# Kernel tuning notes

Hardware: AMD Instinct MI355X
Metric: run time of the kernel (lower is better)

## Reference

```python
import jax, jax.numpy as jnp
import numpy as np

B, S, D = 8, 1024, 1024
NEG = -1e9


def setup_inputs() -> dict:
    key = jax.random.key(0)
    ks = jax.random.split(key, 6)
    context = jax.random.normal(ks[0], (B, S, D), dtype=jnp.float32)
    eos_mask = jax.random.randint(ks[1], (B, S, S), 0, 2).astype(jnp.int32)
    scale = 1.0 / np.sqrt(D).astype(np.float32)
    Wq = jax.random.normal(ks[2], (D, D), dtype=jnp.float32) * scale
    bq = jnp.zeros((D,), jnp.float32)
    Wk = jax.random.normal(ks[3], (D, D), dtype=jnp.float32) * scale
    bk = jnp.zeros((D,), jnp.float32)
    ln_a = jnp.ones((D,), jnp.float32)
    ln_b = jnp.zeros((D,), jnp.float32)
    return dict(context=context, eos_mask=eos_mask, Wq=Wq, bq=bq, Wk=Wk, bk=bk,
                ln_a=ln_a, ln_b=ln_b)


def _forward(context, eos_mask, Wq, bq, Wk, bk, ln_a, ln_b):
    d_model = context.shape[-1]
    seq_len = context.shape[1]
    # LayerNorm with torch-style unbiased std (ddof=1)
    mean = context.mean(-1, keepdims=True)
    var = ((context - mean) ** 2).sum(-1, keepdims=True) / (d_model - 1)
    x = ln_a * (context - mean) / (jnp.sqrt(var) + 1e-6) + ln_b

    a = jnp.eye(seq_len, k=1, dtype=jnp.int32)    # super-diagonal
    b = jnp.eye(seq_len, k=0, dtype=jnp.int32)    # diagonal
    c = jnp.eye(seq_len, k=-1, dtype=jnp.int32)   # sub-diagonal
    tri = jnp.triu(jnp.ones((seq_len, seq_len), jnp.float32), 0)

    mask = eos_mask & (a + c)  # [B,S,S] banded + eos mask

    q = x @ Wq.T + bq
    k = x @ Wk.T + bk
    scores = jnp.einsum('bsd,btd->bst', q, k) / d_model
    scores = jnp.where(mask == 0, NEG, scores)
    neibor = jax.nn.softmax(scores, axis=-1)
    neibor = jnp.sqrt(neibor * jnp.swapaxes(neibor, -2, -1) + 1e-9)

    # log-space triangular matmul 'scan'
    t = jnp.where(a == 0, 0.0, jnp.log(neibor + 1e-9)) @ tri  # [B,S,S]
    g = jnp.exp(jnp.einsum('st,btu->bsu', tri, t))
    strict_upper = tri.astype(jnp.int32) - b
    g = jnp.where(strict_upper == 0, 0.0, g)
    g = g + jnp.swapaxes(g, -2, -1) + jnp.where(b == 0, 1e-9, neibor)
    return g, neibor


def reference(context, eos_mask, Wq, bq, Wk, bk, ln_a, ln_b):
    return _forward(context, eos_mask, Wq, bq, Wk, bk, ln_a, ln_b)
```

## Files before the change

### kernel.cpp

```cpp
#include <hip/hip_runtime.h>
#include <math.h>

#define B_ 8
#define S_ 1024
#define D_ 1024
constexpr int BS = B_ * S_;

typedef short bf16x8 __attribute__((ext_vector_type(8)));
typedef float f32x4 __attribute__((ext_vector_type(4)));

__device__ __forceinline__ unsigned short f2bf(float f) {
    unsigned int u = __float_as_uint(f);
    u += 0x7fffu + ((u >> 16) & 1u);
    return (unsigned short)(u >> 16);
}
__device__ __forceinline__ float bf2f(unsigned short h) {
    return __uint_as_float(((unsigned int)h) << 16);
}

__device__ __forceinline__ float block_reduce_sum(float val, float* sh) {
    int tid = threadIdx.x;
    int lane = tid & 63, w = tid >> 6;
    #pragma unroll
    for (int off = 32; off > 0; off >>= 1) val += __shfl_down(val, off, 64);
    if (lane == 0) sh[w] = val;
    __syncthreads();
    int nw = blockDim.x >> 6;
    float total = 0.f;
    for (int i = 0; i < nw; i++) total += sh[i];
    __syncthreads();
    return total;
}

__global__ void ln_kernel(const float* __restrict__ ctx,
                          const float* __restrict__ ln_a,
                          const float* __restrict__ ln_b,
                          unsigned short* __restrict__ xb) {
    __shared__ float sh[4];
    int r = blockIdx.x;
    int tid = threadIdx.x;
    const float* row = ctx + (size_t)r * D_;
    float v[4];
    float s = 0.f;
    #pragma unroll
    for (int i = 0; i < 4; i++) { v[i] = row[tid + i * 256]; s += v[i]; }
    float total = block_reduce_sum(s, sh);
    float mean = total * (1.0f / D_);
    float sq = 0.f;
    #pragma unroll
    for (int i = 0; i < 4; i++) { float d = v[i] - mean; sq += d * d; }
    float varsum = block_reduce_sum(sq, sh);
    float var = varsum * (1.0f / (D_ - 1));
    float inv = 1.0f / (sqrtf(var) + 1e-6f);
    unsigned short* orow = xb + (size_t)r * D_;
    #pragma unroll
    for (int i = 0; i < 4; i++) {
        int d = tid + i * 256;
        orow[d] = f2bf(ln_a[d] * (v[i] - mean) * inv + ln_b[d]);
    }
}

__global__ void transpose_bf16(const float* __restrict__ in,
                               unsigned short* __restrict__ out, int n) {
    __shared__ float t[32][33];
    int bx = blockIdx.x * 32, by = blockIdx.y * 32;
    int tx = threadIdx.x, ty = threadIdx.y;
    #pragma unroll
    for (int i = 0; i < 32; i += 8)
        t[ty + i][tx] = in[(size_t)(by + ty + i) * n + bx + tx];
    __syncthreads();
    #pragma unroll
    for (int i = 0; i < 32; i += 8)
        out[(size_t)(bx + ty + i) * n + by + tx] = f2bf(t[tx][ty + i]);
}

__global__ __launch_bounds__(256) void gemm_bt(
    const unsigned short* __restrict__ A,
    const unsigned short* __restrict__ Bt,
    unsigned short* __restrict__ C,
    int M, int N, int K) {
    __shared__ __align__(16) unsigned short As[128 * 64];
    __shared__ __align__(16) unsigned short Bs[128 * 64];
    const int tid = threadIdx.x;
    const int wave = tid >> 6, lane = tid & 63;
    const int bm = blockIdx.y * 128, bn = blockIdx.x * 128;
    const int lrow8 = lane >> 3;
    const int pchunk = lane & 7;
    const int m_lane = lane & 15, quad = lane >> 4;
    const int wr = wave >> 1, wc = wave & 1;

    f32x4 acc[4][4] = {};

    for (int k0 = 0; k0 < K; k0 += 64) {
        #pragma unroll
        for (int c = 0; c < 4; c++) {
            int row = wave * 32 + c * 8 + lrow8;
            int gchunk = pchunk ^ (row & 7);
            const unsigned short* gpA = A + (size_t)(bm + row) * K + k0 + gchunk * 8;
            const unsigned short* gpB = Bt + (size_t)(bn + row) * K + k0 + gchunk * 8;
            __builtin_amdgcn_global_load_lds(
                (const __attribute__((address_space(1))) void*)gpA,
                (__attribute__((address_space(3))) void*)(As + (wave * 32 + c * 8) * 64),
                16, 0, 0);
            __builtin_amdgcn_global_load_lds(
                (const __attribute__((address_space(1))) void*)gpB,
                (__attribute__((address_space(3))) void*)(Bs + (wave * 32 + c * 8) * 64),
                16, 0, 0);
        }
        __syncthreads();
        #pragma unroll
        for (int kk = 0; kk < 2; kk++) {
            bf16x8 af[4], bfr[4];
            #pragma unroll
            for (int i = 0; i < 4; i++) {
                int row = wr * 64 + i * 16 + m_lane;
                int lchunk = kk * 4 + quad;
                af[i] = *(const bf16x8*)(As + row * 64 + (lchunk ^ (row & 7)) * 8);
            }
            #pragma unroll
            for (int j = 0; j < 4; j++) {
                int row = wc * 64 + j * 16 + m_lane;
                int lchunk = kk * 4 + quad;
                bfr[j] = *(const bf16x8*)(Bs + row * 64 + (lchunk ^ (row & 7)) * 8);
            }
            #pragma unroll
            for (int i = 0; i < 4; i++)
                #pragma unroll
                for (int j = 0; j < 4; j++)
                    acc[i][j] = __builtin_amdgcn_mfma_f32_16x16x32_bf16(
                        af[i], bfr[j], acc[i][j], 0, 0, 0);
        }
        __syncthreads();
    }
    #pragma unroll
    for (int i = 0; i < 4; i++)
        #pragma unroll
        for (int j = 0; j < 4; j++)
            #pragma unroll
            for (int r = 0; r < 4; r++) {
                int row = bm + wr * 64 + i * 16 + quad * 4 + r;
                int col = bn + wc * 64 + j * 16 + m_lane;
                C[(size_t)row * N + col] = f2bf(acc[i][j][r]);
            }
}

__global__ void bias_terms(const float* __restrict__ Wq, const float* __restrict__ Wk,
                           const float* __restrict__ bq, const float* __restrict__ bk,
                           float* __restrict__ u, float* __restrict__ v,
                           float* __restrict__ c0) {
    __shared__ float sh[4];
    int col = blockIdx.x;
    int tid = threadIdx.x;
    float s = 0.f;
    if (col < D_) {
        for (int d = tid; d < D_; d += 256) s += Wk[(size_t)d * D_ + col] * bq[d];
        s = block_reduce_sum(s, sh);
        if (tid == 0) u[col] = s;
    } else if (col < 2 * D_) {
        int c = col - D_;
        for (int d = tid; d < D_; d += 256) s += Wq[(size_t)d * D_ + c] * bk[d];
        s = block_reduce_sum(s, sh);
        if (tid == 0) v[c] = s;
    } else {
        for (int d = tid; d < D_; d += 256) s += bq[d] * bk[d];
        s = block_reduce_sum(s, sh);
        if (tid == 0) *c0 = s;
    }
}

__global__ void band_dots(const unsigned short* __restrict__ Y,
                          const unsigned short* __restrict__ X,
                          const float* __restrict__ u, const float* __restrict__ v,
                          float* __restrict__ ydu, float* __restrict__ ydd,
                          float* __restrict__ au, float* __restrict__ av) {
    __shared__ float sh[4];
    int r = blockIdx.x;
    int s = r & (S_ - 1);
    int tid = threadIdx.x;
    bool has_up = (s < S_ - 1), has_dn = (s > 0);
    const unsigned short* yrow = Y + (size_t)r * D_;
    const unsigned short* xrow = X + (size_t)r * D_;
    const unsigned short* xup = X + (size_t)(r + 1) * D_;
    const unsigned short* xdn = X + (size_t)(r - 1) * D_;
    int d0 = tid * 4;
    ushort4 yv4 = *(const ushort4*)(yrow + d0);
    ushort4 xv4 = *(const ushort4*)(xrow + d0);
    ushort4 xu4 = has_up ? *(const ushort4*)(xup + d0) : make_ushort4(0, 0, 0, 0);
    ushort4 xd4 = has_dn ? *(const ushort4*)(xdn + d0) : make_ushort4(0, 0, 0, 0);
    float4 uv = *(const float4*)(u + d0);
    float4 vv = *(const float4*)(v + d0);
    float s_up = 0, s_dn = 0, s_u = 0, s_v = 0;
    {
        float y0 = bf2f(yv4.x), y1 = bf2f(yv4.y), y2 = bf2f(yv4.z), y3 = bf2f(yv4.w);
        float x0 = bf2f(xv4.x), x1 = bf2f(xv4.y), x2 = bf2f(xv4.z), x3 = bf2f(xv4.w);
        s_up = y0 * bf2f(xu4.x) + y1 * bf2f(xu4.y) + y2 * bf2f(xu4.z) + y3 * bf2f(xu4.w);
        s_dn = y0 * bf2f(xd4.x) + y1 * bf2f(xd4.y) + y2 * bf2f(xd4.z) + y3 * bf2f(xd4.w);
        s_u = uv.x * x0 + uv.y * x1 + uv.z * x2 + uv.w * x3;
        s_v = vv.x * x0 + vv.y * x1 + vv.z * x2 + vv.w * x3;
    }
    s_up = block_reduce_sum(s_up, sh);
    s_dn = block_reduce_sum(s_dn, sh);
    s_u  = block_reduce_sum(s_u, sh);
    s_v  = block_reduce_sum(s_v, sh);
    if (tid == 0) { ydu[r] = s_up; ydd[r] = s_dn; au[r] = s_u; av[r] = s_v; }
}

__global__ void softmax_band(const float* __restrict__ ydu, const float* __restrict__ ydd,
                             const float* __restrict__ au, const float* __restrict__ av,
                             const float* __restrict__ c0p, const int* __restrict__ eos,
                             float* __restrict__ Pup, float* __restrict__ Pdn,
                             float* __restrict__ bg) {
    int r = blockIdx.x * blockDim.x + threadIdx.x;
    if (r >= BS) return;
    int b = r >> 10, s = r & (S_ - 1);
    float c0 = *c0p;
    const float inv_d = 1.0f / D_;
    bool mu = false, md = false;
    float su = 0.f, sd = 0.f;
    if (s < S_ - 1) {
        mu = eos[(size_t)b * S_ * S_ + (size_t)s * S_ + (s + 1)] != 0;
        su = (ydu[r] + av[r] + au[r + 1] + c0) * inv_d;
    }
    if (s > 0) {
        md = eos[(size_t)b * S_ * S_ + (size_t)s * S_ + (s - 1)] != 0;
        sd = (ydd[r] + av[r] + au[r - 1] + c0) * inv_d;
    }
    float pu, pd, pb;
    if (mu && md) {
        float m = fmaxf(su, sd);
        float eu = expf(su - m), ed = expf(sd - m);
        float inv = 1.0f / (eu + ed);
        pu = eu * inv; pd = ed * inv; pb = 0.f;
    } else if (mu) { pu = 1.f; pd = 0.f; pb = 0.f; }
    else if (md)   { pu = 0.f; pd = 1.f; pb = 0.f; }
    else           { pu = pd = pb = 1.0f / S_; }
    Pup[r] = pu; Pdn[r] = pd; bg[r] = pb;
}

__global__ void prefix_kernel(const float* __restrict__ Pup, const float* __restrict__ Pdn,
                              double* __restrict__ C) {
    __shared__ double wsum[16];
    int b = blockIdx.x;
    int t = threadIdx.x;
    size_t base = (size_t)b * S_;
    double l = 0.0;
    if (t < S_ - 1) {
        float p = sqrtf(Pup[base + t] * Pdn[base + t + 1] + 1e-9f) + 1e-9f;
        l = log((double)p);
    }
    int lane = t & 63, w = t >> 6;
    double v = l;
    #pragma unroll
    for (int off = 1; off < 64; off <<= 1) {
        double o = __shfl_up(v, off, 64);
        if (lane >= off) v += o;
    }
    if (lane == 63) wsum[w] = v;
    __syncthreads();
    if (t == 0) {
        double acc = 0.0;
        #pragma unroll
        for (int i = 0; i < 16; i++) { double x = wsum[i]; wsum[i] = acc; acc += x; }
    }
    __syncthreads();
    v += wsum[w];
    if (t == 0) C[base] = 0.0;
    if (t < S_ - 1) C[base + t + 1] = v;
}

__global__ void write_out(const float* __restrict__ Pup, const float* __restrict__ Pdn,
                          const float* __restrict__ bg, const double* __restrict__ C,
                          float* __restrict__ out) {
    int r = blockIdx.x;
    int b = r >> 10, s = r & (S_ - 1);
    size_t rowbase = (size_t)r * S_;
    size_t bb = (size_t)b * S_;
    float pu_s = (s < S_ - 1) ? Pup[r] : 0.f;
    float pd_s = (s > 0) ? Pdn[r] : 0.f;
    float bg_s = bg[r];
    double C_s = C[r];
    int t0 = threadIdx.x * 4;
    float* gp = out;
    float* np = out + (size_t)B_ * S_ * S_;
    float4 gv, nv;
    #pragma unroll
    for (int j = 0; j < 4; j++) {
        int t = t0 + j;
        float P_st = (t == s + 1) ? pu_s : ((t == s - 1) ? pd_s : bg_s);
        float P_ts;
        if (t == s - 1)      P_ts = Pup[bb + t];
        else if (t == s + 1) P_ts = Pdn[bb + t];
        else                 P_ts = bg[bb + t];
        float neib = sqrtf(P_st * P_ts + 1e-9f);
        float g;
        if (t == s) {
            g = neib;
        } else {
            double diff = (t > s) ? (C[bb + t] - C_s) : (C_s - C[bb + t]);
            g = expf((float)diff) + 1e-9f;
        }
        ((float*)&gv)[j] = g;
        ((float*)&nv)[j] = neib;
    }
    *(float4*)(gp + rowbase + t0) = gv;
    *(float4*)(np + rowbase + t0) = nv;
}

extern "C" void kernel_launch(void* const* d_in, const int* in_sizes, int n_in,
                              void* d_out, int out_size, void* d_ws, size_t ws_size,
                              hipStream_t stream) {
    const float* ctx  = (const float*)d_in[0];
    const int*   eos  = (const int*)d_in[1];
    const float* Wq   = (const float*)d_in[2];
    const float* bq   = (const float*)d_in[3];
    const float* Wk   = (const float*)d_in[4];
    const float* bk   = (const float*)d_in[5];
    const float* ln_a = (const float*)d_in[6];
    const float* ln_b = (const float*)d_in[7];
    float* out = (float*)d_out;

    char* ws = (char*)d_ws;
    size_t off = 0;
    auto alloc = [&](size_t bytes) {
        void* p = ws + off;
        off += (bytes + 255) & ~(size_t)255;
        return p;
    };
    unsigned short* Xb  = (unsigned short*)alloc((size_t)BS * D_ * 2);
    unsigned short* Wqt = (unsigned short*)alloc((size_t)D_ * D_ * 2);
    unsigned short* Wkt = (unsigned short*)alloc((size_t)D_ * D_ * 2);
    unsigned short* Mt  = (unsigned short*)alloc((size_t)D_ * D_ * 2);
    unsigned short* Yb  = (unsigned short*)alloc((size_t)BS * D_ * 2);
    float*  u   = (float*)alloc(D_ * 4);
    float*  v   = (float*)alloc(D_ * 4);
    float*  c0  = (float*)alloc(4);
    float*  ydu = (float*)alloc(BS * 4);
    float*  ydd = (float*)alloc(BS * 4);
    float*  au  = (float*)alloc(BS * 4);
    float*  av  = (float*)alloc(BS * 4);
    float*  Pup = (float*)alloc(BS * 4);
    float*  Pdn = (float*)alloc(BS * 4);
    float*  bg  = (float*)alloc(BS * 4);
    double* Cp  = (double*)alloc(BS * 8);

    ln_kernel<<<BS, 256, 0, stream>>>(ctx, ln_a, ln_b, Xb);
    transpose_bf16<<<dim3(32, 32), dim3(32, 8), 0, stream>>>(Wq, Wqt, D_);
    transpose_bf16<<<dim3(32, 32), dim3(32, 8), 0, stream>>>(Wk, Wkt, D_);
    gemm_bt<<<dim3(8, 8), 256, 0, stream>>>(Wkt, Wqt, Mt, D_, D_, D_);
    bias_terms<<<2 * D_ + 1, 256, 0, stream>>>(Wq, Wk, bq, bk, u, v, c0);
    gemm_bt<<<dim3(8, 64), 256, 0, stream>>>(Xb, Mt, Yb, BS, D_, D_);
    band_dots<<<BS, 256, 0, stream>>>(Yb, Xb, u, v, ydu, ydd, au, av);
    softmax_band<<<BS / 256, 256, 0, stream>>>(ydu, ydd, au, av, c0, eos, Pup, Pdn, bg);
    prefix_kernel<<<B_, 1024, 0, stream>>>(Pup, Pdn, Cp);
    write_out<<<BS, 256, 0, stream>>>(Pup, Pdn, bg, Cp, out);
}
```

Measured before the change: 231.4 us.

## Fuse band dot products into GEMM epilogue and merge small kernels

The big X·M GEMM now computes the banded dot products (Y row against neighbouring X rows, plus the u/v bias terms) in its epilogue. It reduces them with shuffles and atomics, so the bf16 Y intermediate is no longer written and re-read. The two weight transposes share one launch, and bias_terms becomes a row-parallel accumulation with atomics. The weight-product GEMM uses 64x64 tiles for more blocks, and softmax and prefix are merged into one kernel. The atomics need a memset up front, and the epilogue performs scattered global reads of X.

Result: faster. 217.8 us (-5.9%).

```diff
diff --git a/kernel.cpp b/kernel.cpp
--- a/kernel.cpp
+++ b/kernel.cpp
@@ -60,24 +60,127 @@
     }
 }
 
-__global__ void transpose_bf16(const float* __restrict__ in,
-                               unsigned short* __restrict__ out, int n) {
+__global__ void transpose2_bf16(const float* __restrict__ inq,
+                                const float* __restrict__ ink,
+                                unsigned short* __restrict__ outq,
+                                unsigned short* __restrict__ outk) {
     __shared__ float t[32][33];
+    const float* in = blockIdx.z ? ink : inq;
+    unsigned short* out = blockIdx.z ? outk : outq;
     int bx = blockIdx.x * 32, by = blockIdx.y * 32;
     int tx = threadIdx.x, ty = threadIdx.y;
     #pragma unroll
     for (int i = 0; i < 32; i += 8)
-        t[ty + i][tx] = in[(size_t)(by + ty + i) * n + bx + tx];
+        t[ty + i][tx] = in[(size_t)(by + ty + i) * D_ + bx + tx];
     __syncthreads();
     #pragma unroll
     for (int i = 0; i < 32; i += 8)
-        out[(size_t)(bx + ty + i) * n + by + tx] = f2bf(t[tx][ty + i]);
-}
-
-__global__ __launch_bounds__(256) void gemm_bt(
+        out[(size_t)(bx + ty + i) * D_ + by + tx] = f2bf(t[tx][ty + i]);
+}
+
+__global__ void bias_terms(const float* __restrict__ Wq, const float* __restrict__ Wk,
+                           const float* __restrict__ bq, const float* __restrict__ bk,
+                           float* __restrict__ u, float* __restrict__ v,
+                           float* __restrict__ c0) {
+    int b = blockIdx.x;
+    int tid = threadIdx.x;
+    float ua[4] = {}, va[4] = {};
+    int d0 = b * 128;
+    for (int d = d0; d < d0 + 128; d++) {
+        float bqd = bq[d], bkd = bk[d];
+        const float* wkr = Wk + (size_t)d * D_;
+        const float* wqr = Wq + (size_t)d * D_;
+        #pragma unroll
+        for (int i = 0; i < 4; i++) {
+            int c = tid + i * 256;
+            ua[i] += wkr[c] * bqd;
+            va[i] += wqr[c] * bkd;
+        }
+    }
+    #pragma unroll
+    for (int i = 0; i < 4; i++) {
+        atomicAdd(&u[tid + i * 256], ua[i]);
+        atomicAdd(&v[tid + i * 256], va[i]);
+    }
+    if (tid < 128) atomicAdd(c0, bq[d0 + tid] * bk[d0 + tid]);
+}
+
+__global__ __launch_bounds__(256) void gemm_bt64(
     const unsigned short* __restrict__ A,
     const unsigned short* __restrict__ Bt,
     unsigned short* __restrict__ C,
+    int M, int N, int K) {
+    __shared__ __align__(16) unsigned short As[64 * 64];
+    __shared__ __align__(16) unsigned short Bs[64 * 64];
+    const int tid = threadIdx.x;
+    const int wave = tid >> 6, lane = tid & 63;
+    const int bm = blockIdx.y * 64, bn = blockIdx.x * 64;
+    const int lrow8 = lane >> 3;
+    const int pchunk = lane & 7;
+    const int m_lane = lane & 15, quad = lane >> 4;
+    const int wr = wave >> 1, wc = wave & 1;
+
+    f32x4 acc[2][2] = {};
+
+    for (int k0 = 0; k0 < K; k0 += 64) {
+        #pragma unroll
+        for (int c = 0; c < 2; c++) {
+            int row = wave * 16 + c * 8 + lrow8;
+            int gchunk = pchunk ^ (row & 7);
+            const unsigned short* gpA = A + (size_t)(bm + row) * K + k0 + gchunk * 8;
+            const unsigned short* gpB = Bt + (size_t)(bn + row) * K + k0 + gchunk * 8;
+            __builtin_amdgcn_global_load_lds(
+                (const __attribute__((address_space(1))) void*)gpA,
+                (__attribute__((address_space(3))) void*)(As + (wave * 16 + c * 8) * 64),
+                16, 0, 0);
+            __builtin_amdgcn_global_load_lds(
+                (const __attribute__((address_space(1))) void*)gpB,
+                (__attribute__((address_space(3))) void*)(Bs + (wave * 16 + c * 8) * 64),
+                16, 0, 0);
+        }
+        __syncthreads();
+        #pragma unroll
+        for (int kk = 0; kk < 2; kk++) {
+            bf16x8 af[2], bfr[2];
+            #pragma unroll
+            for (int i = 0; i < 2; i++) {
+                int row = wr * 32 + i * 16 + m_lane;
+                int lchunk = kk * 4 + quad;
+                af[i] = *(const bf16x8*)(As + row * 64 + (lchunk ^ (row & 7)) * 8);
+            }
+            #pragma unroll
+            for (int j = 0; j < 2; j++) {
+                int row = wc * 32 + j * 16 + m_lane;
+                int lchunk = kk * 4 + quad;
+                bfr[j] = *(const bf16x8*)(Bs + row * 64 + (lchunk ^ (row & 7)) * 8);
+            }
+            #pragma unroll
+            for (int i = 0; i < 2; i++)
+                #pragma unroll
+                for (int j = 0; j < 2; j++)
+                    acc[i][j] = __builtin_amdgcn_mfma_f32_16x16x32_bf16(
+                        af[i], bfr[j], acc[i][j], 0, 0, 0);
+        }
+        __syncthreads();
+    }
+    #pragma unroll
+    for (int i = 0; i < 2; i++)
+        #pragma unroll
+        for (int j = 0; j < 2; j++)
+            #pragma unroll
+            for (int r = 0; r < 4; r++) {
+                int row = bm + wr * 32 + i * 16 + quad * 4 + r;
+                int col = bn + wc * 32 + j * 16 + m_lane;
+                C[(size_t)row * N + col] = f2bf(acc[i][j][r]);
+            }
+}
+
+__global__ __launch_bounds__(256) void gemm_fused(
+    const unsigned short* __restrict__ A,
+    const unsigned short* __restrict__ Bt,
+    const float* __restrict__ u, const float* __restrict__ v,
+    float* __restrict__ ydu, float* __restrict__ ydd,
+    float* __restrict__ au, float* __restrict__ av,
     int M, int N, int K) {
     __shared__ __align__(16) unsigned short As[128 * 64];
     __shared__ __align__(16) unsigned short Bs[128 * 64];
@@ -132,97 +235,72 @@
         }
         __syncthreads();
     }
-    #pragma unroll
-    for (int i = 0; i < 4; i++)
-        #pragma unroll
-        for (int j = 0; j < 4; j++)
-            #pragma unroll
-            for (int r = 0; r < 4; r++) {
-                int row = bm + wr * 64 + i * 16 + quad * 4 + r;
-                int col = bn + wc * 64 + j * 16 + m_lane;
-                C[(size_t)row * N + col] = f2bf(acc[i][j][r]);
-            }
-}
-
-__global__ void bias_terms(const float* __restrict__ Wq, const float* __restrict__ Wk,
-                           const float* __restrict__ bq, const float* __restrict__ bk,
-                           float* __restrict__ u, float* __restrict__ v,
-                           float* __restrict__ c0) {
-    __shared__ float sh[4];
-    int col = blockIdx.x;
-    int tid = threadIdx.x;
-    float s = 0.f;
-    if (col < D_) {
-        for (int d = tid; d < D_; d += 256) s += Wk[(size_t)d * D_ + col] * bq[d];
-        s = block_reduce_sum(s, sh);
-        if (tid == 0) u[col] = s;
-    } else if (col < 2 * D_) {
-        int c = col - D_;
-        for (int d = tid; d < D_; d += 256) s += Wq[(size_t)d * D_ + c] * bk[d];
-        s = block_reduce_sum(s, sh);
-        if (tid == 0) v[c] = s;
-    } else {
-        for (int d = tid; d < D_; d += 256) s += bq[d] * bk[d];
-        s = block_reduce_sum(s, sh);
-        if (tid == 0) *c0 = s;
-    }
-}
-
-__global__ void band_dots(const unsigned short* __restrict__ Y,
-                          const unsigned short* __restrict__ X,
-                          const float* __restrict__ u, const float* __restrict__ v,
-                          float* __restrict__ ydu, float* __restrict__ ydd,
-                          float* __restrict__ au, float* __restrict__ av) {
-    __shared__ float sh[4];
-    int r = blockIdx.x;
-    int s = r & (S_ - 1);
-    int tid = threadIdx.x;
-    bool has_up = (s < S_ - 1), has_dn = (s > 0);
-    const unsigned short* yrow = Y + (size_t)r * D_;
-    const unsigned short* xrow = X + (size_t)r * D_;
-    const unsigned short* xup = X + (size_t)(r + 1) * D_;
-    const unsigned short* xdn = X + (size_t)(r - 1) * D_;
-    int d0 = tid * 4;
-    ushort4 yv4 = *(const ushort4*)(yrow + d0);
-    ushort4 xv4 = *(const ushort4*)(xrow + d0);
-    ushort4 xu4 = has_up ? *(const ushort4*)(xup + d0) : make_ushort4(0, 0, 0, 0);
-    ushort4 xd4 = has_dn ? *(const ushort4*)(xdn + d0) : make_ushort4(0, 0, 0, 0);
-    float4 uv = *(const float4*)(u + d0);
-    float4 vv = *(const float4*)(v + d0);
-    float s_up = 0, s_dn = 0, s_u = 0, s_v = 0;
-    {
-        float y0 = bf2f(yv4.x), y1 = bf2f(yv4.y), y2 = bf2f(yv4.z), y3 = bf2f(yv4.w);
-        float x0 = bf2f(xv4.x), x1 = bf2f(xv4.y), x2 = bf2f(xv4.z), x3 = bf2f(xv4.w);
-        s_up = y0 * bf2f(xu4.x) + y1 * bf2f(xu4.y) + y2 * bf2f(xu4.z) + y3 * bf2f(xu4.w);
-        s_dn = y0 * bf2f(xd4.x) + y1 * bf2f(xd4.y) + y2 * bf2f(xd4.z) + y3 * bf2f(xd4.w);
-        s_u = uv.x * x0 + uv.y * x1 + uv.z * x2 + uv.w * x3;
-        s_v = vv.x * x0 + vv.y * x1 + vv.z * x2 + vv.w * x3;
-    }
-    s_up = block_reduce_sum(s_up, sh);
-    s_dn = block_reduce_sum(s_dn, sh);
-    s_u  = block_reduce_sum(s_u, sh);
-    s_v  = block_reduce_sum(s_v, sh);
-    if (tid == 0) { ydu[r] = s_up; ydd[r] = s_dn; au[r] = s_u; av[r] = s_v; }
-}
-
-__global__ void softmax_band(const float* __restrict__ ydu, const float* __restrict__ ydd,
-                             const float* __restrict__ au, const float* __restrict__ av,
-                             const float* __restrict__ c0p, const int* __restrict__ eos,
-                             float* __restrict__ Pup, float* __restrict__ Pdn,
-                             float* __restrict__ bg) {
-    int r = blockIdx.x * blockDim.x + threadIdx.x;
-    if (r >= BS) return;
-    int b = r >> 10, s = r & (S_ - 1);
+
+    int cols[4];
+    float uvals[4], vvals[4];
+    #pragma unroll
+    for (int j = 0; j < 4; j++) {
+        cols[j] = bn + wc * 64 + j * 16 + m_lane;
+        uvals[j] = u[cols[j]];
+        vvals[j] = v[cols[j]];
+    }
+    #pragma unroll
+    for (int i = 0; i < 4; i++) {
+        #pragma unroll
+        for (int r = 0; r < 4; r++) {
+            int lrow = wr * 64 + i * 16 + quad * 4 + r;
+            int row = bm + lrow;
+            int s = row & (S_ - 1);
+            bool hu = (s < S_ - 1), hd = (s > 0);
+            const unsigned short* xc = A + (size_t)row * D_;
+            float pu = 0.f, pd = 0.f, pau = 0.f, pav = 0.f;
+            #pragma unroll
+            for (int j = 0; j < 4; j++) {
+                int c = cols[j];
+                float a = acc[i][j][r];
+                float xv = bf2f(xc[c]);
+                if (hu) pu += a * bf2f(xc[c + D_]);
+                if (hd) pd += a * bf2f(xc[c - D_]);
+                pau += uvals[j] * xv;
+                pav += vvals[j] * xv;
+            }
+            #pragma unroll
+            for (int off = 1; off < 16; off <<= 1) {
+                pu += __shfl_xor(pu, off, 64);
+                pd += __shfl_xor(pd, off, 64);
+                pau += __shfl_xor(pau, off, 64);
+                pav += __shfl_xor(pav, off, 64);
+            }
+            if (m_lane == 0) {
+                atomicAdd(&ydu[row], pu);
+                atomicAdd(&ydd[row], pd);
+                atomicAdd(&au[row], pau);
+                atomicAdd(&av[row], pav);
+            }
+        }
+    }
+}
+
+__global__ void softmax_prefix(const float* __restrict__ ydu, const float* __restrict__ ydd,
+                               const float* __restrict__ au, const float* __restrict__ av,
+                               const float* __restrict__ c0p, const int* __restrict__ eos,
+                               float* __restrict__ Pup, float* __restrict__ Pdn,
+                               float* __restrict__ bg, double* __restrict__ C) {
+    __shared__ float pdsh[1024];
+    __shared__ double wsum[16];
+    int b = blockIdx.x;
+    int t = threadIdx.x;
+    int r = b * S_ + t;
     float c0 = *c0p;
     const float inv_d = 1.0f / D_;
     bool mu = false, md = false;
     float su = 0.f, sd = 0.f;
-    if (s < S_ - 1) {
-        mu = eos[(size_t)b * S_ * S_ + (size_t)s * S_ + (s + 1)] != 0;
+    if (t < S_ - 1) {
+        mu = eos[(size_t)b * S_ * S_ + (size_t)t * S_ + (t + 1)] != 0;
         su = (ydu[r] + av[r] + au[r + 1] + c0) * inv_d;
     }
-    if (s > 0) {
-        md = eos[(size_t)b * S_ * S_ + (size_t)s * S_ + (s - 1)] != 0;
+    if (t > 0) {
+        md = eos[(size_t)b * S_ * S_ + (size_t)t * S_ + (t - 1)] != 0;
         sd = (ydd[r] + av[r] + au[r - 1] + c0) * inv_d;
     }
     float pu, pd, pb;
@@ -235,27 +313,21 @@
     else if (md)   { pu = 0.f; pd = 1.f; pb = 0.f; }
     else           { pu = pd = pb = 1.0f / S_; }
     Pup[r] = pu; Pdn[r] = pd; bg[r] = pb;
-}
-
-__global__ void prefix_kernel(const float* __restrict__ Pup, const float* __restrict__ Pdn,
-                              double* __restrict__ C) {
-    __shared__ double wsum[16];
-    int b = blockIdx.x;
-    int t = threadIdx.x;
-    size_t base = (size_t)b * S_;
+    pdsh[t] = pd;
+    __syncthreads();
     double l = 0.0;
     if (t < S_ - 1) {
-        float p = sqrtf(Pup[base + t] * Pdn[base + t + 1] + 1e-9f) + 1e-9f;
+        float p = sqrtf(pu * pdsh[t + 1] + 1e-9f) + 1e-9f;
         l = log((double)p);
     }
     int lane = t & 63, w = t >> 6;
-    double v = l;
+    double vv = l;
     #pragma unroll
     for (int off = 1; off < 64; off <<= 1) {
-        double o = __shfl_up(v, off, 64);
-        if (lane >= off) v += o;
-    }
-    if (lane == 63) wsum[w] = v;
+        double o = __shfl_up(vv, off, 64);
+        if (lane >= off) vv += o;
+    }
+    if (lane == 63) wsum[w] = vv;
     __syncthreads();
     if (t == 0) {
         double acc = 0.0;
@@ -263,9 +335,10 @@
         for (int i = 0; i < 16; i++) { double x = wsum[i]; wsum[i] = acc; acc += x; }
     }
     __syncthreads();
-    v += wsum[w];
+    vv += wsum[w];
+    size_t base = (size_t)b * S_;
     if (t == 0) C[base] = 0.0;
-    if (t < S_ - 1) C[base + t + 1] = v;
+    if (t < S_ - 1) C[base + t + 1] = vv;
 }
 
 __global__ void write_out(const float* __restrict__ Pup, const float* __restrict__ Pdn,
@@ -282,6 +355,7 @@
     int t0 = threadIdx.x * 4;
     float* gp = out;
     float* np = out + (size_t)B_ * S_ * S_;
+    float4 bgv = *(const float4*)(bg + bb + t0);
     float4 gv, nv;
     #pragma unroll
     for (int j = 0; j < 4; j++) {
@@ -290,7 +364,7 @@
         float P_ts;
         if (t == s - 1)      P_ts = Pup[bb + t];
         else if (t == s + 1) P_ts = Pdn[bb + t];
-        else                 P_ts = bg[bb + t];
+        else                 P_ts = ((const float*)&bgv)[j];
         float neib = sqrtf(P_st * P_ts + 1e-9f);
         float g;
         if (t == s) {
@@ -330,27 +404,26 @@
     unsigned short* Wqt = (unsigned short*)alloc((size_t)D_ * D_ * 2);
     unsigned short* Wkt = (unsigned short*)alloc((size_t)D_ * D_ * 2);
     unsigned short* Mt  = (unsigned short*)alloc((size_t)D_ * D_ * 2);
-    unsigned short* Yb  = (unsigned short*)alloc((size_t)BS * D_ * 2);
-    float*  u   = (float*)alloc(D_ * 4);
-    float*  v   = (float*)alloc(D_ * 4);
-    float*  c0  = (float*)alloc(4);
     float*  ydu = (float*)alloc(BS * 4);
     float*  ydd = (float*)alloc(BS * 4);
     float*  au  = (float*)alloc(BS * 4);
     float*  av  = (float*)alloc(BS * 4);
+    float*  u   = (float*)alloc(D_ * 4);
+    float*  v   = (float*)alloc(D_ * 4);
+    float*  c0  = (float*)alloc(4);
+    size_t zero_bytes = (size_t)((char*)c0 - (char*)ydu) + 256;
     float*  Pup = (float*)alloc(BS * 4);
     float*  Pdn = (float*)alloc(BS * 4);
     float*  bg  = (float*)alloc(BS * 4);
     double* Cp  = (double*)alloc(BS * 8);
 
+    hipMemsetAsync(ydu, 0, zero_bytes, stream);
     ln_kernel<<<BS, 256, 0, stream>>>(ctx, ln_a, ln_b, Xb);
-    transpose_bf16<<<dim3(32, 32), dim3(32, 8), 0, stream>>>(Wq, Wqt, D_);
-    transpose_bf16<<<dim3(32, 32), dim3(32, 8), 0, stream>>>(Wk, Wkt, D_);
-    gemm_bt<<<dim3(8, 8), 256, 0, stream>>>(Wkt, Wqt, Mt, D_, D_, D_);
-    bias_terms<<<2 * D_ + 1, 256, 0, stream>>>(Wq, Wk, bq, bk, u, v, c0);
-    gemm_bt<<<dim3(8, 64), 256, 0, stream>>>(Xb, Mt, Yb, BS, D_, D_);
-    band_dots<<<BS, 256, 0, stream>>>(Yb, Xb, u, v, ydu, ydd, au, av);
-    softmax_band<<<BS / 256, 256, 0, stream>>>(ydu, ydd, au, av, c0, eos, Pup, Pdn, bg);
-    prefix_kernel<<<B_, 1024, 0, stream>>>(Pup, Pdn, Cp);
+    transpose2_bf16<<<dim3(32, 32, 2), dim3(32, 8), 0, stream>>>(Wq, Wk, Wqt, Wkt);
+    bias_terms<<<8, 256, 0, stream>>>(Wq, Wk, bq, bk, u, v, c0);
+    gemm_bt64<<<dim3(16, 16), 256, 0, stream>>>(Wkt, Wqt, Mt, D_, D_, D_);
+    gemm_fused<<<dim3(8, 64), 256, 0, stream>>>(Xb, Mt, u, v, ydu, ydd, au, av,
+                                                BS, D_, D_);
+    softmax_prefix<<<B_, 1024, 0, stream>>>(ydu, ydd, au, av, c0, eos, Pup, Pdn, bg, Cp);
     write_out<<<BS, 256, 0, stream>>>(Pup, Pdn, bg, Cp, out);
 }
```
